# Kernel tuning notes

Hardware: AMD Instinct MI355X
Metric: run time of the kernel (lower is better)

Reference implementation:

```python
import jax, jax.numpy as jnp
import numpy as np
from jax import lax

DN = ('NCHW', 'OIHW', 'NCHW')

def conv3x3(x, w):
    return lax.conv_general_dilated(x, w, (1, 1), 'SAME', dimension_numbers=DN)

def conv1x1(x, w, b):
    # w: [O, C], x: [B, C, H, W]
    return jnp.einsum('oc,bchw->bohw', w, x) + b[None, :, None, None]

def bn_relu(x, p):
    # p: [2, C] -> (scale, shift), eval-mode folded BatchNorm + ReLU
    return jax.nn.relu(x * p[0][None, :, None, None] + p[1][None, :, None, None])

def pam(y, Wb, bb, Wc, bc, Wd, bd, alpha):
    B, C, H, W = y.shape
    n = H * W
    b_ = conv1x1(y, Wb, bb).reshape(B, -1, n)   # [B, C/8, N]
    c_ = conv1x1(y, Wc, bc).reshape(B, -1, n)   # [B, C/8, N]
    d_ = conv1x1(y, Wd, bd).reshape(B, C, n)    # [B, C, N]
    energy = jnp.einsum('bkn,bkm->bnm', b_, c_)  # [B, N, N]
    attn = jax.nn.softmax(energy, axis=-1)
    feat = jnp.einsum('bcm,bnm->bcn', d_, attn).reshape(B, C, H, W)
    return alpha[0] * feat + y

def cam(y, beta):
    B, C, H, W = y.shape
    xf = y.reshape(B, C, H * W)
    energy = jnp.einsum('bcn,bdn->bcd', xf, xf)  # [B, C, C]
    energy = jnp.max(energy, axis=-1, keepdims=True) - energy
    attn = jax.nn.softmax(energy, axis=-1)
    feat = jnp.einsum('bcd,bdn->bcn', attn, xf).reshape(B, C, H, W)
    return beta[0] * feat + y

def reference(x, Wp1, bnp1, Wc1, bnc1, Wb, bb, Wc, bc, Wd, bd, alpha, beta,
              Wp2, bnp2, Wc2, bnc2, Wout, bout, Wp3, bp3, Wc3, bc3):
    feat_p = bn_relu(conv3x3(x, Wp1), bnp1)
    feat_p = pam(feat_p, Wb, bb, Wc, bc, Wd, bd, alpha)
    feat_p = bn_relu(conv3x3(feat_p, Wp2), bnp2)

    feat_c = bn_relu(conv3x3(x, Wc1), bnc1)
    feat_c = cam(feat_c, beta)
    feat_c = bn_relu(conv3x3(feat_c, Wc2), bnc2)

    fusion = feat_p + feat_c
    out_main = jax.nn.sigmoid(conv1x1(fusion, Wout, bout))
    out_p = jax.nn.sigmoid(conv1x1(feat_p, Wp3, bp3))
    out_c = jax.nn.sigmoid(conv1x1(feat_c, Wc3, bc3))
    return (out_main, out_p, out_c)

def setup_inputs() -> dict:
    key = jax.random.key(0)
    ks = jax.random.split(key, 24)
    Cin, Ci, Ck, NC = 512, 128, 16, 19
    B, H, W = 8, 64, 64
    s = lambda k, shape, scale=0.05: jax.random.normal(k, shape, jnp.float32) * scale
    return {
        'x': jax.random.normal(ks[0], (B, Cin, H, W), jnp.float32),
        'Wp1': s(ks[1], (Ci, Cin, 3, 3)), 'bnp1': jnp.stack([jnp.ones(Ci), jnp.zeros(Ci)]),
        'Wc1': s(ks[2], (Ci, Cin, 3, 3)), 'bnc1': jnp.stack([jnp.ones(Ci), jnp.zeros(Ci)]),
        'Wb': s(ks[3], (Ck, Ci)), 'bb': s(ks[4], (Ck,)),
        'Wc': s(ks[5], (Ck, Ci)), 'bc': s(ks[6], (Ck,)),
        'Wd': s(ks[7], (Ci, Ci)), 'bd': s(ks[8], (Ci,)),
        'alpha': jax.random.normal(ks[9], (1,), jnp.float32) * 0.5,
        'beta': jax.random.normal(ks[10], (1,), jnp.float32) * 0.5,
        'Wp2': s(ks[11], (Ci, Ci, 3, 3)), 'bnp2': jnp.stack([jnp.ones(Ci), jnp.zeros(Ci)]),
        'Wc2': s(ks[12], (Ci, Ci, 3, 3)), 'bnc2': jnp.stack([jnp.ones(Ci), jnp.zeros(Ci)]),
        'Wout': s(ks[13], (NC, Ci)), 'bout': s(ks[14], (NC,)),
        'Wp3': s(ks[15], (NC, Ci)), 'bp3': s(ks[16], (NC,)),
        'Wc3': s(ks[17], (NC, Ci)), 'bc3': s(ks[18], (NC,)),
    }
```

## Files before the change

### kernel.cpp

```cpp
#include <hip/hip_runtime.h>
#include <math.h>


typedef __attribute__((ext_vector_type(8)))  short short8;
typedef __attribute__((ext_vector_type(16))) float f32x16;

#define GLD_LDS16(gp, lp) __builtin_amdgcn_global_load_lds( \
    (const __attribute__((address_space(1))) void*)(gp),    \
    (__attribute__((address_space(3))) void*)(lp), 16, 0, 0)

__device__ inline unsigned short f2bf(float f) {
    union { float f; unsigned u; } v; v.f = f;
    unsigned r = v.u + 0x7fffu + ((v.u >> 16) & 1u);
    return (unsigned short)(r >> 16);
}
__device__ inline float bf2f(unsigned short h) {
    union { unsigned u; float f; } v; v.u = ((unsigned)h) << 16;
    return v.f;
}

__global__ __launch_bounds__(256) void wpack_kernel(
    const float* __restrict__ W, unsigned short* __restrict__ wp, int Cin, int total)
{
    int idx = blockIdx.x * 256 + threadIdx.x;
    if (idx >= total) return;
    int chunk = idx / 18432;
    int rem   = idx - chunk * 18432;
    int tap   = rem >> 11;
    int rem2  = rem & 2047;
    int g     = rem2 >> 10;
    int co    = (rem2 >> 3) & 127;
    int ci8   = rem2 & 7;
    int cin   = (chunk << 4) + (g << 3) + ci8;
    wp[idx] = f2bf(W[((size_t)co * Cin + cin) * 9 + tap]);
}

__global__ __launch_bounds__(256) void wpack_split_kernel(
    const float* __restrict__ W, unsigned short* __restrict__ wph,
    unsigned short* __restrict__ wpl, int Cin, int total)
{
    int idx = blockIdx.x * 256 + threadIdx.x;
    if (idx >= total) return;
    int chunk = idx / 18432;
    int rem   = idx - chunk * 18432;
    int tap   = rem >> 11;
    int rem2  = rem & 2047;
    int g     = rem2 >> 10;
    int co    = (rem2 >> 3) & 127;
    int ci8   = rem2 & 7;
    int cin   = (chunk << 4) + (g << 3) + ci8;
    float w = W[((size_t)co * Cin + cin) * 9 + tap];
    unsigned short hi = f2bf(w);
    wph[idx] = hi;
    wpl[idx] = f2bf(w - bf2f(hi));
}

__global__ __launch_bounds__(256) void conv3x3_mfma(
    const void* __restrict__ xin, int in_is_fp32, int Cin,
    const unsigned short* __restrict__ wpack, const float* __restrict__ bn,
    float* __restrict__ out_f32, unsigned short* __restrict__ out_bf)
{
    const int t   = threadIdx.x;
    const int w   = t >> 6;
    const int wy  = w >> 1;
    const int wx  = w & 1;
    const int ln  = t & 63;
    const int l31 = ln & 31;
    const int g   = ln >> 5;
    const int y0  = blockIdx.x << 1;
    const int co0 = blockIdx.y << 6;
    const int b   = blockIdx.z;

    __shared__ __align__(16) unsigned short Xl[2 * 264 * 8];
    __shared__ __align__(16) unsigned short Wl[9 * 1024];

    const f32x16 zero = {0,0,0,0,0,0,0,0,0,0,0,0,0,0,0,0};
    f32x16 acc0 = zero, acc1 = zero;

    const int nchunks = Cin >> 4;
    for (int ch = 0; ch < nchunks; ++ch) {
        const int cin0 = ch << 4;
        for (int pid = t; pid < 264; pid += 256) {
            int r  = pid / 66;
            int xc = pid - r * 66;
            int gy = y0 - 1 + r;
            int gx = xc - 1;
            unsigned short tmp[16];
            if ((unsigned)gy < 64u && (unsigned)gx < 64u) {
                if (in_is_fp32) {
                    const float* src = (const float*)xin
                        + (((size_t)b * Cin + cin0) << 12) + (gy << 6) + gx;
#pragma unroll
                    for (int c = 0; c < 16; c++) tmp[c] = f2bf(src[(size_t)c << 12]);
                } else {
                    const unsigned short* src = (const unsigned short*)xin
                        + (((size_t)b * Cin + cin0) << 12) + (gy << 6) + gx;
#pragma unroll
                    for (int c = 0; c < 16; c++) tmp[c] = src[(size_t)c << 12];
                }
            } else {
#pragma unroll
                for (int c = 0; c < 16; c++) tmp[c] = 0;
            }
            *(uint4*)&Xl[(pid << 3)]        = ((uint4*)tmp)[0];
            *(uint4*)&Xl[2112 + (pid << 3)] = ((uint4*)tmp)[1];
        }
        {
            const uint4* wsrc = (const uint4*)wpack;
            const int base = ch * 2304 + co0;
            for (int u0 = (w << 6); u0 < 1152; u0 += 256) {
                const int u = u0 + ln;
                GLD_LDS16(wsrc + base + ((u >> 7) << 8) + (((u >> 6) & 1) << 7) + (u & 63),
                          ((uint4*)Wl) + u0);
            }
        }
        __syncthreads();

#pragma unroll 3
        for (int tap = 0; tap < 9; ++tap) {
            const int dy = tap / 3, dx = tap - dy * 3;
            const int wi = (tap << 10) + (g << 9) + (((wy << 5) + l31) << 3);
            const int row = wx + dy;
            const int xb = ((row * 66 + l31 + dx) << 3) + (g ? 2112 : 0);
            short8 a  = *(const short8*)&Wl[wi];
            short8 b0 = *(const short8*)&Xl[xb];
            short8 b1 = *(const short8*)&Xl[xb + 256];
            acc0 = __builtin_amdgcn_mfma_f32_32x32x16_bf16(a, b0, acc0, 0, 0, 0);
            acc1 = __builtin_amdgcn_mfma_f32_32x32x16_bf16(a, b1, acc1, 0, 0, 0);
        }
        __syncthreads();
    }

    const int y = y0 + wx;
#pragma unroll
    for (int j = 0; j < 2; j++) {
        const f32x16 a = j ? acc1 : acc0;
#pragma unroll
        for (int r = 0; r < 16; r++) {
            int co = co0 + (wy << 5) + (r & 3) + ((r >> 2) << 3) + (g << 2);
            int x  = (j << 5) + l31;
            float v = fmaf(a[r], bn[co], bn[128 + co]);
            v = v > 0.f ? v : 0.f;
            size_t o = (((size_t)b * 128 + co) << 12) + (y << 6) + x;
            if (out_f32) out_f32[o] = v;
            if (out_bf)  out_bf[o]  = f2bf(v);
        }
    }
}

__global__ __launch_bounds__(256) void conv3x3_mfma_hilo(
    const float* __restrict__ xin, int Cin,
    const unsigned short* __restrict__ wph, const unsigned short* __restrict__ wpl,
    const float* __restrict__ bn, float* __restrict__ out_f32,
    unsigned short* __restrict__ outh, unsigned short* __restrict__ outl)
{
    const int t   = threadIdx.x;
    const int w   = t >> 6;
    const int wy  = w >> 1;
    const int wx  = w & 1;
    const int ln  = t & 63;
    const int l31 = ln & 31;
    const int g   = ln >> 5;
    const int y0  = blockIdx.x << 1;
    const int co0 = blockIdx.y << 6;
    const int b   = blockIdx.z;

    __shared__ __align__(16) unsigned short Xh[2 * 264 * 8];
    __shared__ __align__(16) unsigned short Xo[2 * 264 * 8];
    __shared__ __align__(16) unsigned short Wh[9 * 1024];
    __shared__ __align__(16) unsigned short Wo[9 * 1024];

    const f32x16 zero = {0,0,0,0,0,0,0,0,0,0,0,0,0,0,0,0};
    f32x16 acc0 = zero, acc1 = zero;

    const int nchunks = Cin >> 4;
    for (int ch = 0; ch < nchunks; ++ch) {
        const int cin0 = ch << 4;
        for (int pid = t; pid < 264; pid += 256) {
            int r  = pid / 66;
            int xc = pid - r * 66;
            int gy = y0 - 1 + r;
            int gx = xc - 1;
            unsigned short th[16], tl[16];
            if ((unsigned)gy < 64u && (unsigned)gx < 64u) {
                const float* src = xin + (((size_t)b * Cin + cin0) << 12) + (gy << 6) + gx;
#pragma unroll
                for (int c = 0; c < 16; c++) {
                    float f = src[(size_t)c << 12];
                    unsigned short hi = f2bf(f);
                    th[c] = hi;
                    tl[c] = f2bf(f - bf2f(hi));
                }
            } else {
#pragma unroll
                for (int c = 0; c < 16; c++) { th[c] = 0; tl[c] = 0; }
            }
            *(uint4*)&Xh[(pid << 3)]        = ((uint4*)th)[0];
            *(uint4*)&Xh[2112 + (pid << 3)] = ((uint4*)th)[1];
            *(uint4*)&Xo[(pid << 3)]        = ((uint4*)tl)[0];
            *(uint4*)&Xo[2112 + (pid << 3)] = ((uint4*)tl)[1];
        }
        {
            const uint4* sh = (const uint4*)wph;
            const uint4* sl = (const uint4*)wpl;
            const int base = ch * 2304 + co0;
            for (int u0 = (w << 6); u0 < 1152; u0 += 256) {
                const int u = u0 + ln;
                const int o = base + ((u >> 7) << 8) + (((u >> 6) & 1) << 7) + (u & 63);
                GLD_LDS16(sh + o, ((uint4*)Wh) + u0);
                GLD_LDS16(sl + o, ((uint4*)Wo) + u0);
            }
        }
        __syncthreads();

#pragma unroll 1
        for (int tap = 0; tap < 9; ++tap) {
            const int dy = tap / 3, dx = tap - dy * 3;
            const int wi = (tap << 10) + (g << 9) + (((wy << 5) + l31) << 3);
            const int row = wx + dy;
            const int xb = ((row * 66 + l31 + dx) << 3) + (g ? 2112 : 0);
            short8 ah  = *(const short8*)&Wh[wi];
            short8 al  = *(const short8*)&Wo[wi];
            short8 b0h = *(const short8*)&Xh[xb];
            short8 b1h = *(const short8*)&Xh[xb + 256];
            short8 b0l = *(const short8*)&Xo[xb];
            short8 b1l = *(const short8*)&Xo[xb + 256];
            acc0 = __builtin_amdgcn_mfma_f32_32x32x16_bf16(ah, b0h, acc0, 0, 0, 0);
            acc1 = __builtin_amdgcn_mfma_f32_32x32x16_bf16(ah, b1h, acc1, 0, 0, 0);
            acc0 = __builtin_amdgcn_mfma_f32_32x32x16_bf16(ah, b0l, acc0, 0, 0, 0);
            acc1 = __builtin_amdgcn_mfma_f32_32x32x16_bf16(ah, b1l, acc1, 0, 0, 0);
            acc0 = __builtin_amdgcn_mfma_f32_32x32x16_bf16(al, b0h, acc0, 0, 0, 0);
            acc1 = __builtin_amdgcn_mfma_f32_32x32x16_bf16(al, b1h, acc1, 0, 0, 0);
        }
        __syncthreads();
    }

    const int y = y0 + wx;
#pragma unroll
    for (int j = 0; j < 2; j++) {
        const f32x16 a = j ? acc1 : acc0;
#pragma unroll
        for (int r = 0; r < 16; r++) {
            int co = co0 + (wy << 5) + (r & 3) + ((r >> 2) << 3) + (g << 2);
            int x  = (j << 5) + l31;
            float v = fmaf(a[r], bn[co], bn[128 + co]);
            v = v > 0.f ? v : 0.f;
            size_t o = (((size_t)b * 128 + co) << 12) + (y << 6) + x;
            out_f32[o] = v;
            if (outh) {
                unsigned short hi = f2bf(v);
                outh[o] = hi;
                outl[o] = f2bf(v - bf2f(hi));
            }
        }
    }
}

__global__ __launch_bounds__(256) void conv3x3_merged(
    const float* __restrict__ xin,
    const unsigned short* __restrict__ wpp,
    const unsigned short* __restrict__ wph, const unsigned short* __restrict__ wpl,
    const float* __restrict__ bnp, const float* __restrict__ bnc,
    float* __restrict__ outP, float* __restrict__ outC,
    unsigned short* __restrict__ outh, unsigned short* __restrict__ outl)
{
    const int t   = threadIdx.x;
    const int w   = t >> 6;
    const int wy  = w >> 1;
    const int wx  = w & 1;
    const int ln  = t & 63;
    const int l31 = ln & 31;
    const int g   = ln >> 5;
    const int y0  = blockIdx.x << 1;
    const int co0 = blockIdx.y << 6;
    const int b   = blockIdx.z;

    __shared__ __align__(16) unsigned short Xh[2 * 264 * 8];
    __shared__ __align__(16) unsigned short Xo[2 * 264 * 8];
    __shared__ __align__(16) unsigned short Wp[9 * 1024];
    __shared__ __align__(16) unsigned short Wh[9 * 1024];
    __shared__ __align__(16) unsigned short Wo[9 * 1024];

    const f32x16 zero = {0,0,0,0,0,0,0,0,0,0,0,0,0,0,0,0};
    f32x16 ap0 = zero, ap1 = zero, ac0 = zero, ac1 = zero;

    for (int ch = 0; ch < 32; ++ch) {
        const int cin0 = ch << 4;
        for (int pid = t; pid < 264; pid += 256) {
            int r  = pid / 66;
            int xc = pid - r * 66;
            int gy = y0 - 1 + r;
            int gx = xc - 1;
            unsigned short th[16], tl[16];
            if ((unsigned)gy < 64u && (unsigned)gx < 64u) {
                const float* src = xin + (((size_t)b * 512 + cin0) << 12) + (gy << 6) + gx;
#pragma unroll
                for (int c = 0; c < 16; c++) {
                    float f = src[(size_t)c << 12];
                    unsigned short hi = f2bf(f);
                    th[c] = hi;
                    tl[c] = f2bf(f - bf2f(hi));
                }
            } else {
#pragma unroll
                for (int c = 0; c < 16; c++) { th[c] = 0; tl[c] = 0; }
            }
            *(uint4*)&Xh[(pid << 3)]        = ((uint4*)th)[0];
            *(uint4*)&Xh[2112 + (pid << 3)] = ((uint4*)th)[1];
            *(uint4*)&Xo[(pid << 3)]        = ((uint4*)tl)[0];
            *(uint4*)&Xo[2112 + (pid << 3)] = ((uint4*)tl)[1];
        }
        {
            const uint4* sp = (const uint4*)wpp;
            const uint4* sh = (const uint4*)wph;
            const uint4* sl = (const uint4*)wpl;
            const int base = ch * 2304 + co0;
            for (int u0 = (w << 6); u0 < 1152; u0 += 256) {
                const int u = u0 + ln;
                const int o = base + ((u >> 7) << 8) + (((u >> 6) & 1) << 7) + (u & 63);
                GLD_LDS16(sp + o, ((uint4*)Wp) + u0);
                GLD_LDS16(sh + o, ((uint4*)Wh) + u0);
                GLD_LDS16(sl + o, ((uint4*)Wo) + u0);
            }
        }
        __syncthreads();

#pragma unroll 1
        for (int tap = 0; tap < 9; ++tap) {
            const int dy = tap / 3, dx = tap - dy * 3;
            const int wi = (tap << 10) + (g << 9) + (((wy << 5) + l31) << 3);
            const int row = wx + dy;
            const int xb = ((row * 66 + l31 + dx) << 3) + (g ? 2112 : 0);
            short8 vap = *(const short8*)&Wp[wi];
            short8 vah = *(const short8*)&Wh[wi];
            short8 val = *(const short8*)&Wo[wi];
            short8 b0h = *(const short8*)&Xh[xb];
            short8 b1h = *(const short8*)&Xh[xb + 256];
            short8 b0l = *(const short8*)&Xo[xb];
            short8 b1l = *(const short8*)&Xo[xb + 256];
            ap0 = __builtin_amdgcn_mfma_f32_32x32x16_bf16(vap, b0h, ap0, 0, 0, 0);
            ap1 = __builtin_amdgcn_mfma_f32_32x32x16_bf16(vap, b1h, ap1, 0, 0, 0);
            ac0 = __builtin_amdgcn_mfma_f32_32x32x16_bf16(vah, b0h, ac0, 0, 0, 0);
            ac1 = __builtin_amdgcn_mfma_f32_32x32x16_bf16(vah, b1h, ac1, 0, 0, 0);
            ac0 = __builtin_amdgcn_mfma_f32_32x32x16_bf16(vah, b0l, ac0, 0, 0, 0);
            ac1 = __builtin_amdgcn_mfma_f32_32x32x16_bf16(vah, b1l, ac1, 0, 0, 0);
            ac0 = __builtin_amdgcn_mfma_f32_32x32x16_bf16(val, b0h, ac0, 0, 0, 0);
            ac1 = __builtin_amdgcn_mfma_f32_32x32x16_bf16(val, b1h, ac1, 0, 0, 0);
        }
        __syncthreads();
    }

    const int y = y0 + wx;
#pragma unroll
    for (int j = 0; j < 2; j++) {
        const f32x16 aP = j ? ap1 : ap0;
        const f32x16 aC = j ? ac1 : ac0;
#pragma unroll
        for (int r = 0; r < 16; r++) {
            int co = co0 + (wy << 5) + (r & 3) + ((r >> 2) << 3) + (g << 2);
            int x  = (j << 5) + l31;
            size_t o = (((size_t)b * 128 + co) << 12) + (y << 6) + x;
            float vp = fmaf(aP[r], bnp[co], bnp[128 + co]);
            vp = vp > 0.f ? vp : 0.f;
            outP[o] = vp;
            float vc = fmaf(aC[r], bnc[co], bnc[128 + co]);
            vc = vc > 0.f ? vc : 0.f;
            outC[o] = vc;
            unsigned short hi = f2bf(vc);
            outh[o] = hi;
            outl[o] = f2bf(vc - bf2f(hi));
        }
    }
}

__global__ __launch_bounds__(256) void cam_energy_mfma(
    const unsigned short* __restrict__ bh, const unsigned short* __restrict__ bl,
    float* __restrict__ egy_part)
{
    const int t   = threadIdx.x;
    const int w   = t >> 6;
    const int ln  = t & 63;
    const int l31 = ln & 31;
    const int g   = ln >> 5;
    const int i0  = (blockIdx.x >> 2) << 5;
    const int j0  = (blockIdx.x & 3) << 5;
    const int nseg = blockIdx.y;
    const int b   = blockIdx.z;

    __shared__ float red[4][64][17];

    const f32x16 zero = {0,0,0,0,0,0,0,0,0,0,0,0,0,0,0,0};
    f32x16 acc = zero;
    const int nb = (nseg << 9) + (w << 7) + (g << 3);
    const size_t ri = ((size_t)b * 128 + i0 + l31) << 12;
    const size_t rj = ((size_t)b * 128 + j0 + l31) << 12;

#pragma unroll
    for (int c = 0; c < 8; c++) {
        const int n0 = nb + (c << 4);
        short8 ah  = *(const short8*)(bh + ri + n0);
        short8 al  = *(const short8*)(bl + ri + n0);
        short8 bhf = *(const short8*)(bh + rj + n0);
        short8 blf = *(const short8*)(bl + rj + n0);
        acc = __builtin_amdgcn_mfma_f32_32x32x16_bf16(ah, bhf, acc, 0, 0, 0);
        acc = __builtin_amdgcn_mfma_f32_32x32x16_bf16(ah, blf, acc, 0, 0, 0);
        acc = __builtin_amdgcn_mfma_f32_32x32x16_bf16(al, bhf, acc, 0, 0, 0);
    }
#pragma unroll
    for (int r = 0; r < 16; r++) red[w][ln][r] = acc[r];
    __syncthreads();

    const int lane = t & 63;
    const int rq   = t >> 6;
    float* base = egy_part + (((size_t)(nseg * 8 + b)) << 14);
#pragma unroll
    for (int e = 0; e < 4; e++) {
        const int reg = (rq << 2) + e;
        float v = red[0][lane][reg] + red[1][lane][reg]
                + red[2][lane][reg] + red[3][lane][reg];
        const int i = i0 + (reg & 3) + ((reg >> 2) << 3) + ((lane >> 5) << 2);
        base[i * 128 + j0 + (lane & 31)] = v;
    }
}

__global__ __launch_bounds__(256) void cam_softmax_fused(
    const float* __restrict__ egy_part, float* __restrict__ egy)
{
    const int b   = blockIdx.x;
    const int rg  = blockIdx.y;
    const int t   = threadIdx.x;
    const int row = (rg << 4) + (t >> 4);
    const int jg  = t & 15;

    float e[8];
#pragma unroll
    for (int jj = 0; jj < 8; jj++) e[jj] = 0.f;
    for (int seg = 0; seg < 8; seg++) {
        const float* p = egy_part + (((size_t)(seg * 8 + b)) << 14) + row * 128 + (jg << 3);
#pragma unroll
        for (int jj = 0; jj < 8; jj++) e[jj] += p[jj];
    }
    float mn = e[0];
#pragma unroll
    for (int jj = 1; jj < 8; jj++) mn = fminf(mn, e[jj]);
#pragma unroll
    for (int k = 1; k < 16; k <<= 1) mn = fminf(mn, __shfl_xor(mn, k));
    float s = 0.f;
#pragma unroll
    for (int jj = 0; jj < 8; jj++) { float p = __expf(mn - e[jj]); e[jj] = p; s += p; }
#pragma unroll
    for (int k = 1; k < 16; k <<= 1) s += __shfl_xor(s, k);
    const float inv = 1.f / s;
    float* orow = egy + ((size_t)b << 14) + row * 128 + (jg << 3);
// ... 94 lines not shown
    if (L < 32) red[w][L] = mx;
    __syncthreads();
    if (t < 32) {
        float m = fmaxf(fmaxf(red[0][t], red[1][t]), fmaxf(red[2][t], red[3][t]));
        rowmax[((size_t)b << 12) + n0 + t] = m;
    }
}

__global__ __launch_bounds__(256) void pam_attn_mfma(
    const unsigned short* __restrict__ qt, const unsigned short* __restrict__ kt,
    const unsigned short* __restrict__ vb, const float* __restrict__ rowmax,
    const float* __restrict__ alpha, const float* __restrict__ Y,
    unsigned short* __restrict__ outb)
{
    const int t  = threadIdx.x;
    const int w  = t >> 6;
    const int L  = t & 63;
    const int ln = L & 31;
    const int g  = L >> 5;
    const int b  = blockIdx.y;
    const int n0 = blockIdx.x << 5;
    const int c0 = w << 5;

    __shared__ unsigned short Pf[16 * 256];
    __shared__ float red[4][32];

    const f32x16 zero = {0,0,0,0,0,0,0,0,0,0,0,0,0,0,0,0};
    short8 qfrag = *(const short8*)(qt + (((size_t)b * 4096 + n0 + ln) << 4) + (g << 3));
    const float rm = rowmax[((size_t)b << 12) + n0 + ln];
    const float al = alpha[0];

    f32x16 acc = zero;
    float rs = 0.f;

    for (int m0 = 0; m0 < 4096; m0 += 128) {
        const int mq = m0 + (w << 5);
        short8 kfrag = *(const short8*)(kt + (((size_t)b * 4096 + mq + ln) << 4) + (g << 3));
        f32x16 s = __builtin_amdgcn_mfma_f32_32x32x16_bf16(kfrag, qfrag, zero, 0, 0, 0);

        float p[16];
#pragma unroll
        for (int r = 0; r < 16; r++) { p[r] = __expf(s[r] - rm); rs += p[r]; }
        float xx[16];
#pragma unroll
        for (int r = 0; r < 16; r++) xx[r] = __shfl_xor(p[r], 32);

        unsigned short f0[8], f1[8];
#pragma unroll
        for (int i = 0; i < 4; i++) {
            f0[i]     = f2bf(g ? xx[4 + i]  : p[i]);
            f0[4 + i] = f2bf(g ? p[4 + i]   : xx[i]);
            f1[i]     = f2bf(g ? xx[12 + i] : p[8 + i]);
            f1[4 + i] = f2bf(g ? p[12 + i]  : xx[8 + i]);
        }
        *(short8*)(&Pf[((w << 2) + g) * 256 + (ln << 3)])     = *(short8*)f0;
        *(short8*)(&Pf[((w << 2) + 2 + g) * 256 + (ln << 3)]) = *(short8*)f1;
        __syncthreads();

#pragma unroll
        for (int kk = 0; kk < 8; kk++) {
            short8 pfrag = *(const short8*)(&Pf[((kk << 1) + g) * 256 + (ln << 3)]);
            short8 vfrag = *(const short8*)(vb + (((size_t)b * 128 + c0 + ln) << 12)
                                               + m0 + (kk << 4) + (g << 3));
            acc = __builtin_amdgcn_mfma_f32_32x32x16_bf16(vfrag, pfrag, acc, 0, 0, 0);
        }
        __syncthreads();
    }

    rs += __shfl_xor(rs, 32);
    if (L < 32) red[w][L] = rs;
    __syncthreads();
    const float inv = 1.f / (red[0][ln] + red[1][ln] + red[2][ln] + red[3][ln]);
    const int n = n0 + ln;
#pragma unroll
    for (int r = 0; r < 16; r++) {
        int c = c0 + (r & 3) + ((r >> 2) << 3) + (g << 2);
        size_t idx = (((size_t)b * 128 + c) << 12) + n;
        outb[idx] = f2bf(fmaf(al, acc[r] * inv, Y[idx]));
    }
}

__global__ __launch_bounds__(256) void cam_feat(
    const float* __restrict__ attn, const float* __restrict__ Bf,
    const float* __restrict__ beta, float* __restrict__ outf)
{
    const int t  = threadIdx.x;
    const int n  = (blockIdx.x << 8) + t;
    const int c0 = blockIdx.y << 5;
    const int b  = blockIdx.z;
    __shared__ float al[32 * 128];
    for (int idx = t; idx < 4096; idx += 256)
        al[idx] = attn[(size_t)b * 16384 + (c0 + (idx >> 7)) * 128 + (idx & 127)];
    __syncthreads();
    float acc[32];
#pragma unroll
    for (int k = 0; k < 32; k++) acc[k] = 0.f;
    for (int d = 0; d < 128; ++d) {
        float v = Bf[(((size_t)b * 128 + d) << 12) + n];
#pragma unroll
        for (int k = 0; k < 32; k++) acc[k] = fmaf(al[k * 128 + d], v, acc[k]);
    }
    float be = beta[0];
#pragma unroll
    for (int k = 0; k < 32; k++) {
        size_t idx = (((size_t)b * 128 + c0 + k) << 12) + n;
        outf[idx] = fmaf(be, acc[k], Bf[idx]);
    }
}

__global__ __launch_bounds__(256) void heads(
    const float* __restrict__ FP, const float* __restrict__ FC,
    const float* __restrict__ Wout, const float* __restrict__ bout,
    const float* __restrict__ Wp3, const float* __restrict__ bp3,
    const float* __restrict__ Wc3, const float* __restrict__ bc3,
    float* __restrict__ out)
{
    const int t = threadIdx.x;
    const int n = (blockIdx.x << 8) + t;
    const int b = blockIdx.y;
    __shared__ float wl[3 * 19 * 128];
    __shared__ float bl[3 * 19];
    for (int idx = t; idx < 2432; idx += 256) {
        wl[idx]        = Wout[idx];
        wl[2432 + idx] = Wp3[idx];
        wl[4864 + idx] = Wc3[idx];
    }
    if (t < 19) { bl[t] = bout[t]; bl[19 + t] = bp3[t]; bl[38 + t] = bc3[t]; }
    __syncthreads();
    float am[19], ap[19], ac[19];
#pragma unroll
    for (int o = 0; o < 19; o++) { am[o] = 0.f; ap[o] = 0.f; ac[o] = 0.f; }
    for (int chn = 0; chn < 128; ++chn) {
        float pv = FP[(((size_t)b * 128 + chn) << 12) + n];
        float cv = FC[(((size_t)b * 128 + chn) << 12) + n];
        float fv = pv + cv;
#pragma unroll
        for (int o = 0; o < 19; o++) {
            am[o] = fmaf(wl[o * 128 + chn], fv, am[o]);
            ap[o] = fmaf(wl[2432 + o * 128 + chn], pv, ap[o]);
            ac[o] = fmaf(wl[4864 + o * 128 + chn], cv, ac[o]);
        }
    }
    const size_t OS = (size_t)8 * 19 * 4096;
#pragma unroll
    for (int o = 0; o < 19; o++) {
        size_t base = (((size_t)b * 19 + o) << 12) + n;
        out[base]          = 1.f / (1.f + __expf(-(am[o] + bl[o])));
        out[OS + base]     = 1.f / (1.f + __expf(-(ap[o] + bl[19 + o])));
        out[2 * OS + base] = 1.f / (1.f + __expf(-(ac[o] + bl[38 + o])));
    }
}

extern "C" void kernel_launch(void* const* d_in, const int* in_sizes, int n_in,
                              void* d_out, int out_size, void* d_ws, size_t ws_size,
                              hipStream_t stream)
{
    const float* x     = (const float*)d_in[0];
    const float* Wp1   = (const float*)d_in[1];
    const float* bnp1  = (const float*)d_in[2];
    const float* Wc1   = (const float*)d_in[3];
    const float* bnc1  = (const float*)d_in[4];
    const float* Wb    = (const float*)d_in[5];
    const float* bb    = (const float*)d_in[6];
    const float* Wc    = (const float*)d_in[7];
    const float* bcv   = (const float*)d_in[8];
    const float* Wd    = (const float*)d_in[9];
    const float* bd    = (const float*)d_in[10];
    const float* alpha = (const float*)d_in[11];
    const float* beta  = (const float*)d_in[12];
    const float* Wp2   = (const float*)d_in[13];
    const float* bnp2  = (const float*)d_in[14];
    const float* Wc2   = (const float*)d_in[15];
    const float* bnc2  = (const float*)d_in[16];
    const float* Wout  = (const float*)d_in[17];
    const float* bo    = (const float*)d_in[18];
    const float* Wp3   = (const float*)d_in[19];
    const float* bp3   = (const float*)d_in[20];
    const float* Wc3   = (const float*)d_in[21];
    const float* bc3   = (const float*)d_in[22];
    float* out = (float*)d_out;

    char* ws = (char*)d_ws;
    const size_t MB = 1u << 20;
    const size_t W1SZ = (size_t)32 * 18432 * 2;
    const size_t W2SZ = (size_t)8 * 18432 * 2;
    float*          bufA     = (float*)(ws);
    float*          bufB     = (float*)(ws + 16 * MB);
    unsigned short* vb       = (unsigned short*)(ws + 32 * MB);
    float*          egy_part = (float*)(ws + 40 * MB);
    float*          bufD     = (float*)(ws + 32 * MB);
    unsigned short* bh       = (unsigned short*)(ws + 48 * MB);
    unsigned short* blo      = (unsigned short*)(ws + 56 * MB);
    unsigned short* pam_bf   = (unsigned short*)(ws + 48 * MB);
    float*          camf     = (float*)(ws + 48 * MB);
    unsigned short* qt       = (unsigned short*)(ws + 64 * MB);
    unsigned short* kt       = (unsigned short*)(ws + 65 * MB);
    float*          rowmax   = (float*)(ws + 66 * MB);
    float*          egy      = (float*)(ws + 66 * MB + (1u << 17));
    unsigned short* wp1      = (unsigned short*)(ws + 67 * MB);
    unsigned short* wc1h     = (unsigned short*)(ws + 67 * MB + W1SZ);
    unsigned short* wc1l     = (unsigned short*)(ws + 67 * MB + 2 * W1SZ);
    unsigned short* wp2      = (unsigned short*)(ws + 67 * MB + 3 * W1SZ);
    unsigned short* wc2h     = (unsigned short*)(ws + 67 * MB + 3 * W1SZ + W2SZ);
    unsigned short* wc2l     = (unsigned short*)(ws + 67 * MB + 3 * W1SZ + 2 * W2SZ);

    dim3 blk(256);
    const int n1 = 32 * 18432;
    const int n2 = 8 * 18432;
    wpack_kernel<<<dim3((n1 + 255) / 256), blk, 0, stream>>>(Wp1, wp1, 512, n1);
    wpack_kernel<<<dim3((n2 + 255) / 256), blk, 0, stream>>>(Wp2, wp2, 128, n2);
    wpack_split_kernel<<<dim3((n1 + 255) / 256), blk, 0, stream>>>(Wc1, wc1h, wc1l, 512, n1);
    wpack_split_kernel<<<dim3((n2 + 255) / 256), blk, 0, stream>>>(Wc2, wc2h, wc2l, 128, n2);

    conv3x3_merged<<<dim3(32, 2, 8), blk, 0, stream>>>(x, wp1, wc1h, wc1l, bnp1, bnc1,
                                                       bufA, bufB, bh, blo);
    cam_energy_mfma<<<dim3(16, 8, 8), blk, 0, stream>>>(bh, blo, egy_part);
    cam_softmax_fused<<<dim3(8, 8), blk, 0, stream>>>(egy_part, egy);
    pam_qk_1x1<<<dim3(16, 8), blk, 0, stream>>>(bufA, Wb, bb, Wc, bcv, qt, kt);
    pam_v_1x1<<<dim3(16, 4, 8), blk, 0, stream>>>(bufA, Wd, bd, vb);
    pam_rowmax<<<dim3(128, 8), blk, 0, stream>>>(qt, kt, rowmax);
    pam_attn_mfma<<<dim3(128, 8), blk, 0, stream>>>(qt, kt, vb, rowmax, alpha, bufA, pam_bf);
    conv3x3_mfma<<<dim3(32, 2, 8), blk, 0, stream>>>(pam_bf, 0, 128, wp2, bnp2, bufD, (unsigned short*)0);
    cam_feat<<<dim3(16, 4, 8), blk, 0, stream>>>(egy, bufB, beta, camf);
    conv3x3_mfma_hilo<<<dim3(32, 2, 8), blk, 0, stream>>>(camf, 128, wc2h, wc2l, bnc2, bufA,
                                                          (unsigned short*)0, (unsigned short*)0);
    heads<<<dim3(16, 8), blk, 0, stream>>>(bufD, bufA, Wout, bo, Wp3, bp3, Wc3, bc3, out);
}
```

Measured before the change: 816.2 us.

## Double-buffer conv input tiles, read weights from global, pre-split CAM output

All three conv3x3 kernels now double-buffer the activation tile in LDS. The next chunk's input is prefetched into registers while the MFMA loop runs, which cuts one barrier per chunk. Weight fragments are no longer staged through LDS and are loaded straight from global memory (relying on L2/L1 caching), which frees LDS at the cost of more global traffic. cam_feat now writes the bf16 hi/lo split directly, so the second CAM conv reads 16-bit inputs instead of fp32 and skips the per-chunk split.

New measurement: 951.2 us. 1.17x slower.

```diff
diff --git a/kernel.cpp b/kernel.cpp
--- a/kernel.cpp
+++ b/kernel.cpp
@@ -4,10 +4,6 @@
 
 typedef __attribute__((ext_vector_type(8)))  short short8;
 typedef __attribute__((ext_vector_type(16))) float f32x16;
-
-#define GLD_LDS16(gp, lp) __builtin_amdgcn_global_load_lds( \
-    (const __attribute__((address_space(1))) void*)(gp),    \
-    (__attribute__((address_space(3))) void*)(lp), 16, 0, 0)
 
 __device__ inline unsigned short f2bf(float f) {
     union { float f; unsigned u; } v; v.f = f;
@@ -55,10 +51,13 @@
     wpl[idx] = f2bf(w - bf2f(hi));
 }
 
-__global__ __launch_bounds__(256) void conv3x3_mfma(
-    const void* __restrict__ xin, int in_is_fp32, int Cin,
-    const unsigned short* __restrict__ wpack, const float* __restrict__ bn,
-    float* __restrict__ out_f32, unsigned short* __restrict__ out_bf)
+__global__ __launch_bounds__(256) void conv3x3_merged(
+    const float* __restrict__ xin,
+    const unsigned short* __restrict__ wpp,
+    const unsigned short* __restrict__ wph, const unsigned short* __restrict__ wpl,
+    const float* __restrict__ bnp, const float* __restrict__ bnc,
+    float* __restrict__ outP, float* __restrict__ outC,
+    unsigned short* __restrict__ outh, unsigned short* __restrict__ outl)
 {
     const int t   = threadIdx.x;
     const int w   = t >> 6;
@@ -71,88 +70,124 @@
     const int co0 = blockIdx.y << 6;
     const int b   = blockIdx.z;
 
-    __shared__ __align__(16) unsigned short Xl[2 * 264 * 8];
-    __shared__ __align__(16) unsigned short Wl[9 * 1024];
+    const int sr   = t >> 6;
+    const int sx   = t & 63;
+    const int sgy  = y0 - 1 + sr;
+    const bool sv  = (unsigned)sgy < 64u;
+    const int spid = sr * 66 + sx + 1;
+
+    __shared__ __align__(16) unsigned short Xh[2][4224];
+    __shared__ __align__(16) unsigned short Xo[2][4224];
+
+    for (int i = t; i < 1056; i += 256) {
+        uint4 z; z.x = 0; z.y = 0; z.z = 0; z.w = 0;
+        ((uint4*)Xh)[i] = z;
+        ((uint4*)Xo)[i] = z;
+    }
+
+    const int co = co0 + (wy << 5) + l31;
+    const unsigned short* wPb = wpp + (size_t)(g << 10) + ((size_t)co << 3);
+    const unsigned short* wHb = wph + (size_t)(g << 10) + ((size_t)co << 3);
+    const unsigned short* wLb = wpl + (size_t)(g << 10) + ((size_t)co << 3);
+    const float* xsrc = xin + ((size_t)b << 21) + (sgy << 6) + sx;
 
     const f32x16 zero = {0,0,0,0,0,0,0,0,0,0,0,0,0,0,0,0};
-    f32x16 acc0 = zero, acc1 = zero;
-
-    const int nchunks = Cin >> 4;
-    for (int ch = 0; ch < nchunks; ++ch) {
-        const int cin0 = ch << 4;
-        for (int pid = t; pid < 264; pid += 256) {
-            int r  = pid / 66;
-            int xc = pid - r * 66;
-            int gy = y0 - 1 + r;
-            int gx = xc - 1;
-            unsigned short tmp[16];
-            if ((unsigned)gy < 64u && (unsigned)gx < 64u) {
-                if (in_is_fp32) {
-                    const float* src = (const float*)xin
-                        + (((size_t)b * Cin + cin0) << 12) + (gy << 6) + gx;
-#pragma unroll
-                    for (int c = 0; c < 16; c++) tmp[c] = f2bf(src[(size_t)c << 12]);
-                } else {
-                    const unsigned short* src = (const unsigned short*)xin
-                        + (((size_t)b * Cin + cin0) << 12) + (gy << 6) + gx;
-#pragma unroll
-                    for (int c = 0; c < 16; c++) tmp[c] = src[(size_t)c << 12];
-                }
-            } else {
-#pragma unroll
-                for (int c = 0; c < 16; c++) tmp[c] = 0;
-            }
-            *(uint4*)&Xl[(pid << 3)]        = ((uint4*)tmp)[0];
-            *(uint4*)&Xl[2112 + (pid << 3)] = ((uint4*)tmp)[1];
-        }
-        {
-            const uint4* wsrc = (const uint4*)wpack;
-            const int base = ch * 2304 + co0;
-            for (int u0 = (w << 6); u0 < 1152; u0 += 256) {
-                const int u = u0 + ln;
-                GLD_LDS16(wsrc + base + ((u >> 7) << 8) + (((u >> 6) & 1) << 7) + (u & 63),
-                          ((uint4*)Wl) + u0);
-            }
-        }
+    f32x16 ap0 = zero, ap1 = zero, ac0 = zero, ac1 = zero;
+
+    float xv[16];
+    if (sv) {
+#pragma unroll
+        for (int c = 0; c < 16; c++) xv[c] = xsrc[(size_t)c << 12];
+    }
+    __syncthreads();
+
+    if (sv) {
+        unsigned short th[16], tl[16];
+#pragma unroll
+        for (int c = 0; c < 16; c++) {
+            unsigned short hi = f2bf(xv[c]);
+            th[c] = hi; tl[c] = f2bf(xv[c] - bf2f(hi));
+        }
+        *(uint4*)&Xh[0][spid << 3]          = ((uint4*)th)[0];
+        *(uint4*)&Xh[0][2112 + (spid << 3)] = ((uint4*)th)[1];
+        *(uint4*)&Xo[0][spid << 3]          = ((uint4*)tl)[0];
+        *(uint4*)&Xo[0][2112 + (spid << 3)] = ((uint4*)tl)[1];
+    }
+
+    int cur = 0;
+    for (int ch = 0; ch < 32; ++ch) {
         __syncthreads();
-
+        const bool pf = (ch < 31);
+        if (pf && sv) {
+#pragma unroll
+            for (int c = 0; c < 16; c++)
+                xv[c] = xsrc[((size_t)(ch + 1) << 16) + ((size_t)c << 12)];
+        }
+        const size_t wo = (size_t)ch * 18432;
 #pragma unroll 3
         for (int tap = 0; tap < 9; ++tap) {
             const int dy = tap / 3, dx = tap - dy * 3;
-            const int wi = (tap << 10) + (g << 9) + (((wy << 5) + l31) << 3);
             const int row = wx + dy;
-            const int xb = ((row * 66 + l31 + dx) << 3) + (g ? 2112 : 0);
-            short8 a  = *(const short8*)&Wl[wi];
-            short8 b0 = *(const short8*)&Xl[xb];
-            short8 b1 = *(const short8*)&Xl[xb + 256];
-            acc0 = __builtin_amdgcn_mfma_f32_32x32x16_bf16(a, b0, acc0, 0, 0, 0);
-            acc1 = __builtin_amdgcn_mfma_f32_32x32x16_bf16(a, b1, acc1, 0, 0, 0);
-        }
-        __syncthreads();
+            const int xi = (g ? 2112 : 0) + (((row * 66) + l31 + dx) << 3);
+            short8 vap = *(const short8*)(wPb + wo + tap * 2048);
+            short8 vah = *(const short8*)(wHb + wo + tap * 2048);
+            short8 val = *(const short8*)(wLb + wo + tap * 2048);
+            short8 b0h = *(const short8*)&Xh[cur][xi];
+            short8 b1h = *(const short8*)&Xh[cur][xi + 256];
+            short8 b0l = *(const short8*)&Xo[cur][xi];
+            short8 b1l = *(const short8*)&Xo[cur][xi + 256];
+            ap0 = __builtin_amdgcn_mfma_f32_32x32x16_bf16(vap, b0h, ap0, 0, 0, 0);
+            ap1 = __builtin_amdgcn_mfma_f32_32x32x16_bf16(vap, b1h, ap1, 0, 0, 0);
+            ac0 = __builtin_amdgcn_mfma_f32_32x32x16_bf16(vah, b0h, ac0, 0, 0, 0);
+            ac1 = __builtin_amdgcn_mfma_f32_32x32x16_bf16(vah, b1h, ac1, 0, 0, 0);
+            ac0 = __builtin_amdgcn_mfma_f32_32x32x16_bf16(vah, b0l, ac0, 0, 0, 0);
+            ac1 = __builtin_amdgcn_mfma_f32_32x32x16_bf16(vah, b1l, ac1, 0, 0, 0);
+            ac0 = __builtin_amdgcn_mfma_f32_32x32x16_bf16(val, b0h, ac0, 0, 0, 0);
+            ac1 = __builtin_amdgcn_mfma_f32_32x32x16_bf16(val, b1h, ac1, 0, 0, 0);
+        }
+        if (pf && sv) {
+            unsigned short th[16], tl[16];
+#pragma unroll
+            for (int c = 0; c < 16; c++) {
+                unsigned short hi = f2bf(xv[c]);
+                th[c] = hi; tl[c] = f2bf(xv[c] - bf2f(hi));
+            }
+            const int nb = cur ^ 1;
+            *(uint4*)&Xh[nb][spid << 3]          = ((uint4*)th)[0];
+            *(uint4*)&Xh[nb][2112 + (spid << 3)] = ((uint4*)th)[1];
+            *(uint4*)&Xo[nb][spid << 3]          = ((uint4*)tl)[0];
+            *(uint4*)&Xo[nb][2112 + (spid << 3)] = ((uint4*)tl)[1];
+        }
+        cur ^= 1;
     }
 
     const int y = y0 + wx;
 #pragma unroll
     for (int j = 0; j < 2; j++) {
-        const f32x16 a = j ? acc1 : acc0;
+        const f32x16 aP = j ? ap1 : ap0;
+        const f32x16 aC = j ? ac1 : ac0;
 #pragma unroll
         for (int r = 0; r < 16; r++) {
-            int co = co0 + (wy << 5) + (r & 3) + ((r >> 2) << 3) + (g << 2);
+            int c2 = co0 + (wy << 5) + (r & 3) + ((r >> 2) << 3) + (g << 2);
             int x  = (j << 5) + l31;
-            float v = fmaf(a[r], bn[co], bn[128 + co]);
-            v = v > 0.f ? v : 0.f;
-            size_t o = (((size_t)b * 128 + co) << 12) + (y << 6) + x;
-            if (out_f32) out_f32[o] = v;
-            if (out_bf)  out_bf[o]  = f2bf(v);
-        }
-    }
-}
-
-__global__ __launch_bounds__(256) void conv3x3_mfma_hilo(
-    const float* __restrict__ xin, int Cin,
-    const unsigned short* __restrict__ wph, const unsigned short* __restrict__ wpl,
-    const float* __restrict__ bn, float* __restrict__ out_f32,
-    unsigned short* __restrict__ outh, unsigned short* __restrict__ outl)
+            size_t o = (((size_t)b * 128 + c2) << 12) + (y << 6) + x;
+            float vp = fmaf(aP[r], bnp[c2], bnp[128 + c2]);
+            vp = vp > 0.f ? vp : 0.f;
+            outP[o] = vp;
+            float vc = fmaf(aC[r], bnc[c2], bnc[128 + c2]);
+            vc = vc > 0.f ? vc : 0.f;
+            outC[o] = vc;
+            unsigned short hi = f2bf(vc);
+            outh[o] = hi;
+            outl[o] = f2bf(vc - bf2f(hi));
+        }
+    }
+}
+
+__global__ __launch_bounds__(256) void conv3x3_bf(
+    const unsigned short* __restrict__ xin, int Cin,
+    const unsigned short* __restrict__ wpk, const float* __restrict__ bn,
+    float* __restrict__ out_f32)
 {
     const int t   = threadIdx.x;
     const int w   = t >> 6;
@@ -165,74 +200,66 @@
     const int co0 = blockIdx.y << 6;
     const int b   = blockIdx.z;
 
-    __shared__ __align__(16) unsigned short Xh[2 * 264 * 8];
-    __shared__ __align__(16) unsigned short Xo[2 * 264 * 8];
-    __shared__ __align__(16) unsigned short Wh[9 * 1024];
-    __shared__ __align__(16) unsigned short Wo[9 * 1024];
+    const int sr   = t >> 6;
+    const int sx   = t & 63;
+    const int sgy  = y0 - 1 + sr;
+    const bool sv  = (unsigned)sgy < 64u;
+    const int spid = sr * 66 + sx + 1;
+
+    __shared__ __align__(16) unsigned short Xl[2][4224];
+
+    for (int i = t; i < 1056; i += 256) {
+        uint4 z; z.x = 0; z.y = 0; z.z = 0; z.w = 0;
+        ((uint4*)Xl)[i] = z;
+    }
+
+    const int co = co0 + (wy << 5) + l31;
+    const unsigned short* wB = wpk + (size_t)(g << 10) + ((size_t)co << 3);
+    const unsigned short* xsrc = xin + (((size_t)b * Cin) << 12) + (sgy << 6) + sx;
 
     const f32x16 zero = {0,0,0,0,0,0,0,0,0,0,0,0,0,0,0,0};
     f32x16 acc0 = zero, acc1 = zero;
 
+    unsigned short xv[16];
+    if (sv) {
+#pragma unroll
+        for (int c = 0; c < 16; c++) xv[c] = xsrc[(size_t)c << 12];
+    }
+    __syncthreads();
+
+    if (sv) {
+        *(uint4*)&Xl[0][spid << 3]          = ((uint4*)xv)[0];
+        *(uint4*)&Xl[0][2112 + (spid << 3)] = ((uint4*)xv)[1];
+    }
+
     const int nchunks = Cin >> 4;
+    int cur = 0;
     for (int ch = 0; ch < nchunks; ++ch) {
-        const int cin0 = ch << 4;
-        for (int pid = t; pid < 264; pid += 256) {
-            int r  = pid / 66;
-            int xc = pid - r * 66;
-            int gy = y0 - 1 + r;
-            int gx = xc - 1;
-            unsigned short th[16], tl[16];
-            if ((unsigned)gy < 64u && (unsigned)gx < 64u) {
-                const float* src = xin + (((size_t)b * Cin + cin0) << 12) + (gy << 6) + gx;
-#pragma unroll
-                for (int c = 0; c < 16; c++) {
-                    float f = src[(size_t)c << 12];
-                    unsigned short hi = f2bf(f);
-                    th[c] = hi;
-                    tl[c] = f2bf(f - bf2f(hi));
-                }
-            } else {
-#pragma unroll
-                for (int c = 0; c < 16; c++) { th[c] = 0; tl[c] = 0; }
-            }
-            *(uint4*)&Xh[(pid << 3)]        = ((uint4*)th)[0];
-            *(uint4*)&Xh[2112 + (pid << 3)] = ((uint4*)th)[1];
-            *(uint4*)&Xo[(pid << 3)]        = ((uint4*)tl)[0];
-            *(uint4*)&Xo[2112 + (pid << 3)] = ((uint4*)tl)[1];
-        }
-        {
-            const uint4* sh = (const uint4*)wph;
-            const uint4* sl = (const uint4*)wpl;
-            const int base = ch * 2304 + co0;
-            for (int u0 = (w << 6); u0 < 1152; u0 += 256) {
-                const int u = u0 + ln;
-                const int o = base + ((u >> 7) << 8) + (((u >> 6) & 1) << 7) + (u & 63);
-                GLD_LDS16(sh + o, ((uint4*)Wh) + u0);
-                GLD_LDS16(sl + o, ((uint4*)Wo) + u0);
-            }
-        }
         __syncthreads();
-
-#pragma unroll 1
+        const bool pf = (ch < nchunks - 1);
+        if (pf && sv) {
+#pragma unroll
+            for (int c = 0; c < 16; c++)
+                xv[c] = xsrc[((size_t)(ch + 1) << 16) + ((size_t)c << 12)];
+        }
+        const size_t wo = (size_t)ch * 18432;
+#pragma unroll 3
         for (int tap = 0; tap < 9; ++tap) {
             const int dy = tap / 3, dx = tap - dy * 3;
-            const int wi = (tap << 10) + (g << 9) + (((wy << 5) + l31) << 3);
             const int row = wx + dy;
-            const int xb = ((row * 66 + l31 + dx) << 3) + (g ? 2112 : 0);
-            short8 ah  = *(const short8*)&Wh[wi];
-            short8 al  = *(const short8*)&Wo[wi];
-            short8 b0h = *(const short8*)&Xh[xb];
-            short8 b1h = *(const short8*)&Xh[xb + 256];
-            short8 b0l = *(const short8*)&Xo[xb];
-            short8 b1l = *(const short8*)&Xo[xb + 256];
-            acc0 = __builtin_amdgcn_mfma_f32_32x32x16_bf16(ah, b0h, acc0, 0, 0, 0);
-            acc1 = __builtin_amdgcn_mfma_f32_32x32x16_bf16(ah, b1h, acc1, 0, 0, 0);
-            acc0 = __builtin_amdgcn_mfma_f32_32x32x16_bf16(ah, b0l, acc0, 0, 0, 0);
-            acc1 = __builtin_amdgcn_mfma_f32_32x32x16_bf16(ah, b1l, acc1, 0, 0, 0);
-            acc0 = __builtin_amdgcn_mfma_f32_32x32x16_bf16(al, b0h, acc0, 0, 0, 0);
-            acc1 = __builtin_amdgcn_mfma_f32_32x32x16_bf16(al, b1h, acc1, 0, 0, 0);
-        }
-        __syncthreads();
+            const int xi = (g ? 2112 : 0) + (((row * 66) + l31 + dx) << 3);
+            short8 a  = *(const short8*)(wB + wo + tap * 2048);
+            short8 b0 = *(const short8*)&Xl[cur][xi];
+            short8 b1 = *(const short8*)&Xl[cur][xi + 256];
+            acc0 = __builtin_amdgcn_mfma_f32_32x32x16_bf16(a, b0, acc0, 0, 0, 0);
+            acc1 = __builtin_amdgcn_mfma_f32_32x32x16_bf16(a, b1, acc1, 0, 0, 0);
+        }
+        if (pf && sv) {
+            const int nb = cur ^ 1;
+            *(uint4*)&Xl[nb][spid << 3]          = ((uint4*)xv)[0];
+            *(uint4*)&Xl[nb][2112 + (spid << 3)] = ((uint4*)xv)[1];
+        }
+        cur ^= 1;
     }
 
     const int y = y0 + wx;
@@ -241,28 +268,19 @@
         const f32x16 a = j ? acc1 : acc0;
 #pragma unroll
         for (int r = 0; r < 16; r++) {
-            int co = co0 + (wy << 5) + (r & 3) + ((r >> 2) << 3) + (g << 2);
+            int c2 = co0 + (wy << 5) + (r & 3) + ((r >> 2) << 3) + (g << 2);
             int x  = (j << 5) + l31;
-            float v = fmaf(a[r], bn[co], bn[128 + co]);
+            float v = fmaf(a[r], bn[c2], bn[128 + c2]);
             v = v > 0.f ? v : 0.f;
-            size_t o = (((size_t)b * 128 + co) << 12) + (y << 6) + x;
-            out_f32[o] = v;
-            if (outh) {
-                unsigned short hi = f2bf(v);
-                outh[o] = hi;
-                outl[o] = f2bf(v - bf2f(hi));
-            }
-        }
-    }
-}
-
-__global__ __launch_bounds__(256) void conv3x3_merged(
-    const float* __restrict__ xin,
-    const unsigned short* __restrict__ wpp,
-    const unsigned short* __restrict__ wph, const unsigned short* __restrict__ wpl,
-    const float* __restrict__ bnp, const float* __restrict__ bnc,
-    float* __restrict__ outP, float* __restrict__ outC,
-    unsigned short* __restrict__ outh, unsigned short* __restrict__ outl)
+            out_f32[(((size_t)b * 128 + c2) << 12) + (y << 6) + x] = v;
+        }
+    }
+}
+
+__global__ __launch_bounds__(256) void conv3x3_hilo_bf(
+    const unsigned short* __restrict__ xhg, const unsigned short* __restrict__ xlg,
+    int Cin, const unsigned short* __restrict__ wph, const unsigned short* __restrict__ wpl,
+    const float* __restrict__ bn, float* __restrict__ out_f32)
 {
     const int t   = threadIdx.x;
     const int w   = t >> 6;
@@ -275,100 +293,96 @@
     const int co0 = blockIdx.y << 6;
     const int b   = blockIdx.z;
 
-    __shared__ __align__(16) unsigned short Xh[2 * 264 * 8];
-    __shared__ __align__(16) unsigned short Xo[2 * 264 * 8];
-    __shared__ __align__(16) unsigned short Wp[9 * 1024];
-    __shared__ __align__(16) unsigned short Wh[9 * 1024];
-    __shared__ __align__(16) unsigned short Wo[9 * 1024];
+    const int sr   = t >> 6;
+    const int sx   = t & 63;
+    const int sgy  = y0 - 1 + sr;
+    const bool sv  = (unsigned)sgy < 64u;
+    const int spid = sr * 66 + sx + 1;
+
+    __shared__ __align__(16) unsigned short Xh[2][4224];
+    __shared__ __align__(16) unsigned short Xo[2][4224];
+
+    for (int i = t; i < 1056; i += 256) {
+        uint4 z; z.x = 0; z.y = 0; z.z = 0; z.w = 0;
+        ((uint4*)Xh)[i] = z;
+        ((uint4*)Xo)[i] = z;
+    }
+
+    const int co = co0 + (wy << 5) + l31;
+    const unsigned short* wHb = wph + (size_t)(g << 10) + ((size_t)co << 3);
+    const unsigned short* wLb = wpl + (size_t)(g << 10) + ((size_t)co << 3);
+    const unsigned short* hsrc = xhg + (((size_t)b * Cin) << 12) + (sgy << 6) + sx;
+    const unsigned short* lsrc = xlg + (((size_t)b * Cin) << 12) + (sgy << 6) + sx;
 
     const f32x16 zero = {0,0,0,0,0,0,0,0,0,0,0,0,0,0,0,0};
-    f32x16 ap0 = zero, ap1 = zero, ac0 = zero, ac1 = zero;
-
-    for (int ch = 0; ch < 32; ++ch) {
-        const int cin0 = ch << 4;
-        for (int pid = t; pid < 264; pid += 256) {
-            int r  = pid / 66;
-            int xc = pid - r * 66;
-            int gy = y0 - 1 + r;
-            int gx = xc - 1;
-            unsigned short th[16], tl[16];
-            if ((unsigned)gy < 64u && (unsigned)gx < 64u) {
-                const float* src = xin + (((size_t)b * 512 + cin0) << 12) + (gy << 6) + gx;
-#pragma unroll
-                for (int c = 0; c < 16; c++) {
-                    float f = src[(size_t)c << 12];
-                    unsigned short hi = f2bf(f);
-                    th[c] = hi;
-                    tl[c] = f2bf(f - bf2f(hi));
-                }
-            } else {
-#pragma unroll
-                for (int c = 0; c < 16; c++) { th[c] = 0; tl[c] = 0; }
+    f32x16 acc0 = zero, acc1 = zero;
+
+    unsigned short hv[16], lv[16];
+    if (sv) {
+#pragma unroll
+        for (int c = 0; c < 16; c++) { hv[c] = hsrc[(size_t)c << 12]; lv[c] = lsrc[(size_t)c << 12]; }
+    }
+    __syncthreads();
+
+    if (sv) {
+        *(uint4*)&Xh[0][spid << 3]          = ((uint4*)hv)[0];
+        *(uint4*)&Xh[0][2112 + (spid << 3)] = ((uint4*)hv)[1];
+        *(uint4*)&Xo[0][spid << 3]          = ((uint4*)lv)[0];
+        *(uint4*)&Xo[0][2112 + (spid << 3)] = ((uint4*)lv)[1];
+    }
+
+    const int nchunks = Cin >> 4;
+    int cur = 0;
+    for (int ch = 0; ch < nchunks; ++ch) {
+        __syncthreads();
+        const bool pf = (ch < nchunks - 1);
+        if (pf && sv) {
+#pragma unroll
+            for (int c = 0; c < 16; c++) {
+                hv[c] = hsrc[((size_t)(ch + 1) << 16) + ((size_t)c << 12)];
+                lv[c] = lsrc[((size_t)(ch + 1) << 16) + ((size_t)c << 12)];
             }
-            *(uint4*)&Xh[(pid << 3)]        = ((uint4*)th)[0];
-            *(uint4*)&Xh[2112 + (pid << 3)] = ((uint4*)th)[1];
-            *(uint4*)&Xo[(pid << 3)]        = ((uint4*)tl)[0];
-            *(uint4*)&Xo[2112 + (pid << 3)] = ((uint4*)tl)[1];
-        }
-        {
-            const uint4* sp = (const uint4*)wpp;
-            const uint4* sh = (const uint4*)wph;
-            const uint4* sl = (const uint4*)wpl;
-            const int base = ch * 2304 + co0;
-            for (int u0 = (w << 6); u0 < 1152; u0 += 256) {
-                const int u = u0 + ln;
-                const int o = base + ((u >> 7) << 8) + (((u >> 6) & 1) << 7) + (u & 63);
-                GLD_LDS16(sp + o, ((uint4*)Wp) + u0);
-                GLD_LDS16(sh + o, ((uint4*)Wh) + u0);
-                GLD_LDS16(sl + o, ((uint4*)Wo) + u0);
-            }
-        }
-        __syncthreads();
-
-#pragma unroll 1
+        }
+        const size_t wo = (size_t)ch * 18432;
+#pragma unroll 3
         for (int tap = 0; tap < 9; ++tap) {
             const int dy = tap / 3, dx = tap - dy * 3;
-            const int wi = (tap << 10) + (g << 9) + (((wy << 5) + l31) << 3);
             const int row = wx + dy;
-            const int xb = ((row * 66 + l31 + dx) << 3) + (g ? 2112 : 0);
-            short8 vap = *(const short8*)&Wp[wi];
-            short8 vah = *(const short8*)&Wh[wi];
-            short8 val = *(const short8*)&Wo[wi];
-            short8 b0h = *(const short8*)&Xh[xb];
-            short8 b1h = *(const short8*)&Xh[xb + 256];
-            short8 b0l = *(const short8*)&Xo[xb];
-            short8 b1l = *(const short8*)&Xo[xb + 256];
-            ap0 = __builtin_amdgcn_mfma_f32_32x32x16_bf16(vap, b0h, ap0, 0, 0, 0);
-            ap1 = __builtin_amdgcn_mfma_f32_32x32x16_bf16(vap, b1h, ap1, 0, 0, 0);
-            ac0 = __builtin_amdgcn_mfma_f32_32x32x16_bf16(vah, b0h, ac0, 0, 0, 0);
-            ac1 = __builtin_amdgcn_mfma_f32_32x32x16_bf16(vah, b1h, ac1, 0, 0, 0);
-            ac0 = __builtin_amdgcn_mfma_f32_32x32x16_bf16(vah, b0l, ac0, 0, 0, 0);
-            ac1 = __builtin_amdgcn_mfma_f32_32x32x16_bf16(vah, b1l, ac1, 0, 0, 0);
-            ac0 = __builtin_amdgcn_mfma_f32_32x32x16_bf16(val, b0h, ac0, 0, 0, 0);
-            ac1 = __builtin_amdgcn_mfma_f32_32x32x16_bf16(val, b1h, ac1, 0, 0, 0);
-        }
-        __syncthreads();
+            const int xi = (g ? 2112 : 0) + (((row * 66) + l31 + dx) << 3);
+            short8 ah  = *(const short8*)(wHb + wo + tap * 2048);
+            short8 al  = *(const short8*)(wLb + wo + tap * 2048);
+            short8 b0h = *(const short8*)&Xh[cur][xi];
+            short8 b1h = *(const short8*)&Xh[cur][xi + 256];
+            short8 b0l = *(const short8*)&Xo[cur][xi];
+            short8 b1l = *(const short8*)&Xo[cur][xi + 256];
+            acc0 = __builtin_amdgcn_mfma_f32_32x32x16_bf16(ah, b0h, acc0, 0, 0, 0);
+            acc1 = __builtin_amdgcn_mfma_f32_32x32x16_bf16(ah, b1h, acc1, 0, 0, 0);
+            acc0 = __builtin_amdgcn_mfma_f32_32x32x16_bf16(ah, b0l, acc0, 0, 0, 0);
+            acc1 = __builtin_amdgcn_mfma_f32_32x32x16_bf16(ah, b1l, acc1, 0, 0, 0);
+            acc0 = __builtin_amdgcn_mfma_f32_32x32x16_bf16(al, b0h, acc0, 0, 0, 0);
+            acc1 = __builtin_amdgcn_mfma_f32_32x32x16_bf16(al, b1h, acc1, 0, 0, 0);
+        }
+        if (pf && sv) {
+            const int nb = cur ^ 1;
+            *(uint4*)&Xh[nb][spid << 3]          = ((uint4*)hv)[0];
+            *(uint4*)&Xh[nb][2112 + (spid << 3)] = ((uint4*)hv)[1];
+            *(uint4*)&Xo[nb][spid << 3]          = ((uint4*)lv)[0];
+            *(uint4*)&Xo[nb][2112 + (spid << 3)] = ((uint4*)lv)[1];
+        }
+        cur ^= 1;
     }
 
     const int y = y0 + wx;
 #pragma unroll
     for (int j = 0; j < 2; j++) {
-        const f32x16 aP = j ? ap1 : ap0;
-        const f32x16 aC = j ? ac1 : ac0;
+        const f32x16 a = j ? acc1 : acc0;
 #pragma unroll
         for (int r = 0; r < 16; r++) {
-            int co = co0 + (wy << 5) + (r & 3) + ((r >> 2) << 3) + (g << 2);
+            int c2 = co0 + (wy << 5) + (r & 3) + ((r >> 2) << 3) + (g << 2);
             int x  = (j << 5) + l31;
-            size_t o = (((size_t)b * 128 + co) << 12) + (y << 6) + x;
-            float vp = fmaf(aP[r], bnp[co], bnp[128 + co]);
-            vp = vp > 0.f ? vp : 0.f;
-            outP[o] = vp;
-            float vc = fmaf(aC[r], bnc[co], bnc[128 + co]);
-            vc = vc > 0.f ? vc : 0.f;
-            outC[o] = vc;
-            unsigned short hi = f2bf(vc);
-            outh[o] = hi;
-            outl[o] = f2bf(vc - bf2f(hi));
+            float v = fmaf(a[r], bn[c2], bn[128 + c2]);
+            v = v > 0.f ? v : 0.f;
+            out_f32[(((size_t)b * 128 + c2) << 12) + (y << 6) + x] = v;
         }
     }
 }
@@ -629,7 +643,8 @@
 
 __global__ __launch_bounds__(256) void cam_feat(
     const float* __restrict__ attn, const float* __restrict__ Bf,
-    const float* __restrict__ beta, float* __restrict__ outf)
+    const float* __restrict__ beta, unsigned short* __restrict__ oh,
+    unsigned short* __restrict__ ol)
 {
     const int t  = threadIdx.x;
     const int n  = (blockIdx.x << 8) + t;
@@ -651,7 +666,10 @@
 #pragma unroll
     for (int k = 0; k < 32; k++) {
         size_t idx = (((size_t)b * 128 + c0 + k) << 12) + n;
-        outf[idx] = fmaf(be, acc[k], Bf[idx]);
+        float v = fmaf(be, acc[k], Bf[idx]);
+        unsigned short hi = f2bf(v);
+        oh[idx] = hi;
+        ol[idx] = f2bf(v - bf2f(hi));
     }
 }
 
@@ -739,7 +757,8 @@
     unsigned short* bh       = (unsigned short*)(ws + 48 * MB);
     unsigned short* blo      = (unsigned short*)(ws + 56 * MB);
     unsigned short* pam_bf   = (unsigned short*)(ws + 48 * MB);
-    float*          camf     = (float*)(ws + 48 * MB);
+    unsigned short* c2h      = (unsigned short*)(ws + 48 * MB);
+    unsigned short* c2l      = (unsigned short*)(ws + 56 * MB);
     unsigned short* qt       = (unsigned short*)(ws + 64 * MB);
     unsigned short* kt       = (unsigned short*)(ws + 65 * MB);
     float*          rowmax   = (float*)(ws + 66 * MB);
@@ -767,9 +786,8 @@
     pam_v_1x1<<<dim3(16, 4, 8), blk, 0, stream>>>(bufA, Wd, bd, vb);
     pam_rowmax<<<dim3(128, 8), blk, 0, stream>>>(qt, kt, rowmax);
     pam_attn_mfma<<<dim3(128, 8), blk, 0, stream>>>(qt, kt, vb, rowmax, alpha, bufA, pam_bf);
-    conv3x3_mfma<<<dim3(32, 2, 8), blk, 0, stream>>>(pam_bf, 0, 128, wp2, bnp2, bufD, (unsigned short*)0);
-    cam_feat<<<dim3(16, 4, 8), blk, 0, stream>>>(egy, bufB, beta, camf);
-    conv3x3_mfma_hilo<<<dim3(32, 2, 8), blk, 0, stream>>>(camf, 128, wc2h, wc2l, bnc2, bufA,
-                                                          (unsigned short*)0, (unsigned short*)0);
+    conv3x3_bf<<<dim3(32, 2, 8), blk, 0, stream>>>(pam_bf, 128, wp2, bnp2, bufD);
+    cam_feat<<<dim3(16, 4, 8), blk, 0, stream>>>(egy, bufB, beta, c2h, c2l);
+    conv3x3_hilo_bf<<<dim3(32, 2, 8), blk, 0, stream>>>(c2h, c2l, 128, wc2h, wc2l, bnc2, bufA);
     heads<<<dim3(16, 8), blk, 0, stream>>>(bufD, bufA, Wout, bo, Wp3, bp3, Wc3, bc3, out);
 }
```
